# Kernel tuning notes

Hardware: AMD Instinct MI355X
Metric: run time of the kernel (lower is better)

## Reference

```python
import jax, jax.numpy as jnp
import numpy as np

N_DELTA, N_THETA, N_GAMMA = 64, 128, 512
N_TOTAL = N_DELTA + N_THETA + N_GAMMA  # 704
N_CLASSES = 1000
N_STEPS = 5
DT = 0.01
COUPLING = 2.0      # coupling_strength
PAC_DT = 0.3        # delta->theta phase-amplitude coupling depth
PAC_TG = 0.3        # theta->gamma phase-amplitude coupling depth
SPARSITY = 0.1      # PhaseToRateConverter sparsity (fraction of active units)
SHARP = 10.0        # softness of the 'soft' sparsification gate
TWO_PI = 2.0 * np.pi
B = 65536


def setup_inputs() -> dict:
    key = jax.random.key(0)
    k1, k2, k3, k4 = jax.random.split(key, 4)
    x = jax.random.normal(k1, (B, N_TOTAL), dtype=jnp.float32)
    # per-sample random initial phases in [0,1), scaled to [0,2pi) inside reference
    phase0 = jax.random.uniform(k2, (B, N_TOTAL), dtype=jnp.float32)
    W = jax.random.normal(k3, (N_CLASSES, N_TOTAL), dtype=jnp.float32) * 0.02
    b = jax.random.normal(k4, (N_CLASSES,), dtype=jnp.float32) * 0.02
    return {"x": x, "phase0": phase0, "W": W, "b": b}


def _kuramoto(phi):
    # mean-field within-band Kuramoto coupling: K * mean_j sin(phi_j - phi_i)
    S = jnp.mean(jnp.sin(phi), axis=-1, keepdims=True)
    C = jnp.mean(jnp.cos(phi), axis=-1, keepdims=True)
    return COUPLING * (S * jnp.cos(phi) - C * jnp.sin(phi))


def _mean_phase(phi):
    # circular mean phase of a band, shape (B,1)
    return jnp.arctan2(jnp.mean(jnp.sin(phi), axis=-1, keepdims=True),
                       jnp.mean(jnp.cos(phi), axis=-1, keepdims=True))


def _forward(x, phase0, W, b):
    freqs = jnp.concatenate([
        jnp.linspace(1.0, 4.0, N_DELTA),    # delta band Hz
        jnp.linspace(4.0, 8.0, N_THETA),    # theta band Hz
        jnp.linspace(30.0, 80.0, N_GAMMA),  # gamma band Hz
    ]).astype(x.dtype)
    phi = phase0 * TWO_PI                       # (B, N_TOTAL)
    amp = 1.0 + jnp.abs(x) * 0.01               # amplitude seeded by |x|*0.01 on unit base
    d = slice(0, N_DELTA)
    t = slice(N_DELTA, N_DELTA + N_THETA)
    g = slice(N_DELTA + N_THETA, N_TOTAL)

    def step(carry, _):
        phi, amp = carry
        dphi = TWO_PI * freqs + jnp.concatenate(
            [_kuramoto(phi[:, d]), _kuramoto(phi[:, t]), _kuramoto(phi[:, g])], axis=-1)
        psi_d = _mean_phase(phi[:, d])
        psi_t = _mean_phase(phi[:, t])
        # PAC: theta amplitude driven by delta phase, gamma amplitude by theta phase
        damp = jnp.concatenate([
            jnp.zeros_like(amp[:, d]),
            PAC_DT * amp[:, t] * jnp.cos(psi_d),
            PAC_TG * amp[:, g] * jnp.cos(psi_t),
        ], axis=-1)
        phi_new = jnp.mod(phi + DT * dphi, TWO_PI)
        amp_new = amp + DT * damp
        return (phi_new, amp_new), None

    (phi, amp), _ = jax.lax.scan(step, (phi, amp), None, length=N_STEPS)

    # PhaseToRateConverter, mode='soft': raw rate then soft top-(sparsity) gate
    raw = amp * 0.5 * (1.0 + jnp.cos(phi))                              # (B, N_TOTAL)
    thr = jnp.quantile(raw, 1.0 - SPARSITY, axis=-1, keepdims=True)    # per-sample threshold
    rate = raw * jax.nn.sigmoid((raw - thr) * SHARP)
    return rate @ W.T + b                                               # (B, N_CLASSES)


def reference(x, phase0, W, b):
    return _forward(x, phase0, W, b)
```

## Files before the change

### kernel.cpp

```cpp
#include <hip/hip_runtime.h>

#define NB 65536
#define NTOT 704
#define NCLS 1000
#define NPAD 1024
#define KDIM 704

typedef __attribute__((ext_vector_type(8))) short bf16x8;
typedef __attribute__((ext_vector_type(4))) float f32x4;
typedef __attribute__((ext_vector_type(2))) float f32x2;

#define WB_ELEMS (NPAD * KDIM)
#define LUT_DC_OFF (2u * (WB_ELEMS + 46137344u))
#define LUT_DS_OFF (LUT_DC_OFF + NTOT * 4u)

__device__ __forceinline__ f32x2 sp(float x) { return (f32x2){x, x}; }

template <int CTRL>
__device__ __forceinline__ float dpp_shuf(float v) {
  return __int_as_float(__builtin_amdgcn_update_dpp(0, __float_as_int(v), CTRL, 0xF, 0xF, true));
}
__device__ __forceinline__ float swz16(float v) {
  return __int_as_float(__builtin_amdgcn_ds_swizzle(__float_as_int(v), 0x401F));
}
__device__ __forceinline__ float wsum_f(float v) {
  v += dpp_shuf<0xB1>(v);
  v += dpp_shuf<0x4E>(v);
  v += dpp_shuf<0x141>(v);
  v += dpp_shuf<0x140>(v);
  v += swz16(v);
  v += __shfl_xor(v, 32, 64);
  return v;
}
__device__ __forceinline__ float wmax_f(float v) {
  v = fmaxf(v, dpp_shuf<0xB1>(v));
  v = fmaxf(v, dpp_shuf<0x4E>(v));
  v = fmaxf(v, dpp_shuf<0x141>(v));
  v = fmaxf(v, dpp_shuf<0x140>(v));
  v = fmaxf(v, swz16(v));
  v = fmaxf(v, __shfl_xor(v, 32, 64));
  return v;
}
__device__ __forceinline__ float wmin_f(float v) {
  v = fminf(v, dpp_shuf<0xB1>(v));
  v = fminf(v, dpp_shuf<0x4E>(v));
  v = fminf(v, dpp_shuf<0x141>(v));
  v = fminf(v, dpp_shuf<0x140>(v));
  v = fminf(v, swz16(v));
  v = fminf(v, __shfl_xor(v, 32, 64));
  return v;
}

__device__ __forceinline__ unsigned short f2bf(float v) {
  unsigned u = __float_as_uint(v);
  u = (u + 0x7FFFu + ((u >> 16) & 1u)) >> 16;
  return (unsigned short)u;
}

__global__ __launch_bounds__(256) void convw_kernel(const float* __restrict__ W,
                                                    unsigned short* __restrict__ Wb,
                                                    float* __restrict__ dcL,
                                                    float* __restrict__ dsL) {
  int i = blockIdx.x * 256 + threadIdx.x;
  if (i < NTOT) {
    float f;
    if (i < 64)       f = 1.0f + 3.0f * (float)i * (1.0f / 63.0f);
    else if (i < 192) f = 4.0f + 4.0f * (float)(i - 64) * (1.0f / 127.0f);
    else              f = 30.0f + 50.0f * (float)(i - 192) * (1.0f / 511.0f);
    const float rev = 0.01f * f;
    dcL[i] = __builtin_amdgcn_cosf(rev);
    dsL[i] = __builtin_amdgcn_sinf(rev);
  }
  if (i >= NPAD * KDIM) return;
  int n = i / KDIM;
  float v = (n < NCLS) ? W[i] : 0.0f;
  Wb[i] = f2bf(v);
}

__global__ __launch_bounds__(256) void sim_kernel(const float* __restrict__ x,
                                                  const float* __restrict__ p0,
                                                  const float* __restrict__ dcL,
                                                  const float* __restrict__ dsL,
                                                  unsigned short* __restrict__ rateb) {
  const int wave = threadIdx.x >> 6;
  const int lane = threadIdx.x & 63;
  const int sample = blockIdx.x * 4 + wave;
  const size_t base = (size_t)sample * NTOT;

  float sD, cD, ampD, dcD, dsD;
  f32x2 sPp[5], cPp[5], dc2[5], ds2[5], amp2[5];
  {
    const float p = p0[base + lane];
    sD = __builtin_amdgcn_sinf(p);
    cD = __builtin_amdgcn_cosf(p);
    ampD = fmaf(fabsf(x[base + lane]), 0.01f, 1.0f);
    dcD = dcL[lane]; dsD = dsL[lane];
  }
#pragma unroll
  for (int pr = 0; pr < 5; ++pr) {
    const int i0 = (1 + 2 * pr) * 64 + lane;
    const int i1 = i0 + 64;
    const float pa = p0[base + i0], pb = p0[base + i1];
    sPp[pr] = (f32x2){__builtin_amdgcn_sinf(pa), __builtin_amdgcn_sinf(pb)};
    cPp[pr] = (f32x2){__builtin_amdgcn_cosf(pa), __builtin_amdgcn_cosf(pb)};
    amp2[pr] = (f32x2){fmaf(fabsf(x[base + i0]), 0.01f, 1.0f),
                       fmaf(fabsf(x[base + i1]), 0.01f, 1.0f)};
    dc2[pr] = (f32x2){dcL[i0], dcL[i1]};
    ds2[pr] = (f32x2){dsL[i0], dsL[i1]};
  }

  float prodT = 1.0f, prodG = 1.0f;

#pragma unroll
  for (int st = 0; st < 5; ++st) {
    const float Sd = wsum_f(sD);
    const float Cd = wsum_f(cD);
    const float St = wsum_f(sPp[0].x + sPp[0].y);
    const float Ct = wsum_f(cPp[0].x + cPp[0].y);
    const f32x2 gs = (sPp[1] + sPp[2]) + (sPp[3] + sPp[4]);
    const f32x2 gc = (cPp[1] + cPp[2]) + (cPp[3] + cPp[4]);
    const float Sg = wsum_f(gs.x + gs.y);
    const float Cg = wsum_f(gc.x + gc.y);
    const float cpd = Cd * __builtin_amdgcn_rsqf(fmaf(Sd, Sd, Cd * Cd));
    const float cpt = Ct * __builtin_amdgcn_rsqf(fmaf(St, St, Ct * Ct));
    prodT *= fmaf(0.003f, cpd, 1.0f);
    prodG *= fmaf(0.003f, cpt, 1.0f);
    const float sdm = Sd * (0.02f / 64.0f),  cdm = Cd * (0.02f / 64.0f);
    const float stm = St * (0.02f / 128.0f), ctm = Ct * (0.02f / 128.0f);
    const float sgm = Sg * (0.02f / 512.0f), cgm = Cg * (0.02f / 512.0f);
    {
      const float eps = fmaf(-cdm, sD, sdm * cD);
      const float e2 = eps * eps;
      const float ce = fmaf(-0.5f, e2, 1.0f);
      const float cd_ = fmaf(-dsD, eps, dcD * ce);
      const float sd_ = fmaf(dcD, eps, dsD * ce);
      const float sn = fmaf(cD, sd_, sD * cd_);
      const float cn = fmaf(-sD, sd_, cD * cd_);
      sD = sn; cD = cn;
    }
#pragma unroll
    for (int pr = 0; pr < 5; ++pr) {
      const f32x2 Sm = sp(pr == 0 ? stm : sgm);
      const f32x2 Cm = sp(pr == 0 ? ctm : cgm);
      const f32x2 s2 = sPp[pr], c2 = cPp[pr];
      const f32x2 eps = Sm * c2 - Cm * s2;
      const f32x2 e2 = eps * eps;
      const f32x2 ce = sp(1.0f) - sp(0.5f) * e2;
      const f32x2 cosd = dc2[pr] * ce - ds2[pr] * eps;
      const f32x2 sind = ds2[pr] * ce + dc2[pr] * eps;
      sPp[pr] = s2 * cosd + c2 * sind;
      cPp[pr] = c2 * cosd - s2 * sind;
    }
  }

  float raw[11];
  unsigned kk[11];
  {
    const float h = 0.5f * ampD;
    raw[0] = fmaf(h, cD, h);
  }
  const float hT = 0.5f * prodT, hG = 0.5f * prodG;
#pragma unroll
  for (int pr = 0; pr < 5; ++pr) {
    const f32x2 h2 = amp2[pr] * sp(pr == 0 ? hT : hG);
    const f32x2 r2 = h2 * cPp[pr] + h2;
    raw[1 + 2 * pr] = r2.x;
    raw[2 + 2 * pr] = r2.y;
  }
#pragma unroll
  for (int e = 0; e < 11; ++e) kk[e] = (unsigned)(raw[e] * 8192.0f);

  unsigned pre = 0;
#pragma unroll
  for (int bit = 13; bit >= 0; --bit) {
    const unsigned u = pre | ((1u << bit) - 1u);
    int cnt = 0;
#pragma unroll
    for (int e = 0; e < 11; ++e) cnt += (int)__popcll(__ballot(kk[e] <= u));
    if (cnt < 633) pre |= (1u << bit);
  }

  int clt = 0, ceq = 0;
#pragma unroll
  for (int e = 0; e < 11; ++e) {
    clt += (int)__popcll(__ballot(kk[e] < pre));
    ceq += (int)__popcll(__ballot(kk[e] == pre));
  }

  const float qv = 0.9f * 703.0f;
  float thr;
  if (clt + ceq >= 634) {
    thr = ((float)pre + 0.5f) * (1.0f / 8192.0f);
  } else {
    float mx = -1.0f, mn = 3.0e38f;
#pragma unroll
    for (int e = 0; e < 11; ++e) {
      mx = fmaxf(mx, (kk[e] == pre) ? raw[e] : -1.0f);
      mn = fminf(mn, (kk[e] > pre) ? raw[e] : 3.0e38f);
    }
    const float S632 = wmax_f(mx);
    const float S633 = wmin_f(mn);
    thr = S632 * (633.0f - qv) + S633 * (qv - 632.0f);
  }

#pragma unroll
  for (int e = 0; e < 11; ++e) {
    const float r = raw[e];
    const float t = __expf((thr - r) * 10.0f);
    const float sg = __builtin_amdgcn_rcpf(1.0f + t);
    rateb[base + e * 64 + lane] = f2bf(r * sg);
  }
}

#define BM 128
#define BN 128
#define BK 64
#define NKT (KDIM / BK)

__device__ __forceinline__ void gload16(const unsigned short* g, unsigned short* l) {
  __builtin_amdgcn_global_load_lds((const __attribute__((address_space(1))) void*)g,
                                   (__attribute__((address_space(3))) void*)l,
                                   16, 0, 0);
}

__global__ __launch_bounds__(256) void gemm_kernel(const unsigned short* __restrict__ A,
                                                   const unsigned short* __restrict__ Bw,
                                                   const float* __restrict__ bias,
                                                   float* __restrict__ C) {
  __shared__ unsigned short lA[2][BM * BK];
  __shared__ unsigned short lB[2][BN * BK];
  const int tid  = threadIdx.x;
  const int wave = tid >> 6;
  const int lane = tid & 63;

  const int bid = blockIdx.x;
  const int swz = (bid & 7) * 512 + (bid >> 3);
  const int bm = swz >> 3;
  const int bn = swz & 7;

  const int wr = wave >> 1;
  const int wc = wave & 1;

  f32x4 acc[4][4];
#pragma unroll
  for (int i = 0; i < 4; ++i)
#pragma unroll
    for (int j = 0; j < 4; ++j) acc[i][j] = (f32x4){0.f, 0.f, 0.f, 0.f};

  const int lrow  = lane >> 3;
  const int lkblk = (((lane & 7) ^ lrow)) * 8;

  const unsigned short* Abase = A  + (size_t)(bm * BM) * KDIM;
  const unsigned short* Bbase = Bw + (size_t)(bn * BN) * KDIM;

#define STAGE(buf, kt)                                                          \
  {                                                                             \
    const int k0_ = (kt) * BK;                                                  \
    _Pragma("unroll")                                                           \
    for (int i_ = 0; i_ < 4; ++i_) {                                            \
      const int c_ = wave * 4 + i_;                                             \
      gload16(Abase + (size_t)(c_ * 8 + lrow) * KDIM + k0_ + lkblk,             \
              &lA[buf][c_ * 512]);                                              \
      gload16(Bbase + (size_t)(c_ * 8 + lrow) * KDIM + k0_ + lkblk,             \
              &lB[buf][c_ * 512]);                                              \
    }                                                                           \
  }

  STAGE(0, 0);
  __syncthreads();

  int buf = 0;
  for (int kt = 0; kt < NKT; ++kt) {
    if (kt < NKT - 1) STAGE(buf ^ 1, kt + 1);
#pragma unroll
    for (int ks = 0; ks < 2; ++ks) {
      bf16x8 av[4], bv[4];
      const int slot = 8 * ((((ks << 2) | (lane >> 4)) ^ (lane & 7)));
#pragma unroll
      for (int m = 0; m < 4; ++m) {
        const int r = wr * 64 + m * 16 + (lane & 15);
        av[m] = *(const bf16x8*)&lA[buf][r * BK + slot];
      }
#pragma unroll
      for (int n = 0; n < 4; ++n) {
        const int r = wc * 64 + n * 16 + (lane & 15);
        bv[n] = *(const bf16x8*)&lB[buf][r * BK + slot];
      }
#pragma unroll
      for (int m = 0; m < 4; ++m)
#pragma unroll
        for (int n = 0; n < 4; ++n)
          acc[m][n] = __builtin_amdgcn_mfma_f32_16x16x32_bf16(av[m], bv[n], acc[m][n], 0, 0, 0);
    }
    __syncthreads();
    buf ^= 1;
  }

  const int crow0 = bm * BM + wr * 64;
  const int ccol0 = bn * BN + wc * 64;
  const int rql = (lane >> 4) * 4;
  const int cl  = lane & 15;
#pragma unroll
  for (int n = 0; n < 4; ++n) {
    const int col = ccol0 + n * 16 + cl;
    if (col < NCLS) {
      const float bb = bias[col];
#pragma unroll
      for (int m = 0; m < 4; ++m) {
#pragma unroll
        for (int r = 0; r < 4; ++r) {
          const int row = crow0 + m * 16 + rql + r;
          C[(size_t)row * NCLS + col] = acc[m][n][r] + bb;
        }
      }
    }
  }
}

extern "C" void kernel_launch(void* const* d_in, const int* in_sizes, int n_in,
                              void* d_out, int out_size, void* d_ws, size_t ws_size,
                              hipStream_t stream) {
  const float* x    = (const float*)d_in[0];
  const float* p0   = (const float*)d_in[1];
  const float* W    = (const float*)d_in[2];
  const float* bias = (const float*)d_in[3];
  float* out = (float*)d_out;

  unsigned short* Wb    = (unsigned short*)d_ws;
  unsigned short* rateb = (unsigned short*)d_ws + WB_ELEMS;
  float* dcL = (float*)((char*)d_ws + LUT_DC_OFF);
  float* dsL = (float*)((char*)d_ws + LUT_DS_OFF);

  convw_kernel<<<dim3((NPAD * KDIM + 255) / 256), dim3(256), 0, stream>>>(W, Wb, dcL, dsL);
  sim_kernel<<<dim3(NB / 4), dim3(256), 0, stream>>>(x, p0, dcL, dsL, rateb);
  gemm_kernel<<<dim3((NB / BM) * (NPAD / BN)), dim3(256), 0, stream>>>(rateb, Wb, bias, out);
}
```

Before: 362.4 us.

## Software-pipeline GEMM main loop with register fragments and two-deep prefetch

Restructures the bf16 GEMM main loop so each iteration first reads all LDS fragments for both k-substeps into registers. It then frees that buffer with a barrier and issues the global-to-LDS loads for tile kt+2 into it, so those loads overlap the MFMA work. Hand-written s_waitcnt vmcnt/lgkmcnt and s_barrier instructions replace __syncthreads, and the last two tiles are peeled into an epilogue. In exchange, register pressure rises because twice as many fragments are held, and correctness now depends on the hand-placed wait counts.

```diff
diff --git a/kernel.cpp b/kernel.cpp
--- a/kernel.cpp
+++ b/kernel.cpp
@@ -223,12 +223,46 @@
                                    16, 0, 0);
 }
 
+struct Frags {
+  bf16x8 a[2][4];
+  bf16x8 b[2][4];
+};
+
+__device__ __forceinline__ void read_frags(Frags& f,
+                                           const unsigned short* la,
+                                           const unsigned short* lb,
+                                           int wr, int wc, int lane) {
+  const int l15 = lane & 15;
+  const int s0 = 8 * (((lane >> 4)) ^ (lane & 7));
+  const int s1 = 8 * ((4 | (lane >> 4)) ^ (lane & 7));
+#pragma unroll
+  for (int m = 0; m < 4; ++m) {
+    const int rA = (wr * 64 + m * 16 + l15) * BK;
+    const int rB = (wc * 64 + m * 16 + l15) * BK;
+    f.a[0][m] = *(const bf16x8*)&la[rA + s0];
+    f.a[1][m] = *(const bf16x8*)&la[rA + s1];
+    f.b[0][m] = *(const bf16x8*)&lb[rB + s0];
+    f.b[1][m] = *(const bf16x8*)&lb[rB + s1];
+  }
+}
+
+__device__ __forceinline__ void do_mfma(const Frags& f, f32x4 acc[4][4]) {
+#pragma unroll
+  for (int ks = 0; ks < 2; ++ks)
+#pragma unroll
+    for (int m = 0; m < 4; ++m)
+#pragma unroll
+      for (int n = 0; n < 4; ++n)
+        acc[m][n] = __builtin_amdgcn_mfma_f32_16x16x32_bf16(f.a[ks][m], f.b[ks][n],
+                                                            acc[m][n], 0, 0, 0);
+}
+
 __global__ __launch_bounds__(256) void gemm_kernel(const unsigned short* __restrict__ A,
                                                    const unsigned short* __restrict__ Bw,
                                                    const float* __restrict__ bias,
                                                    float* __restrict__ C) {
-  __shared__ unsigned short lA[2][BM * BK];
-  __shared__ unsigned short lB[2][BN * BK];
+  __shared__ __align__(16) unsigned short lA[2][BM * BK];
+  __shared__ __align__(16) unsigned short lB[2][BN * BK];
   const int tid  = threadIdx.x;
   const int wave = tid >> 6;
   const int lane = tid & 63;
@@ -267,34 +301,30 @@
   }
 
   STAGE(0, 0);
-  __syncthreads();
-
-  int buf = 0;
-  for (int kt = 0; kt < NKT; ++kt) {
-    if (kt < NKT - 1) STAGE(buf ^ 1, kt + 1);
-#pragma unroll
-    for (int ks = 0; ks < 2; ++ks) {
-      bf16x8 av[4], bv[4];
-      const int slot = 8 * ((((ks << 2) | (lane >> 4)) ^ (lane & 7)));
-#pragma unroll
-      for (int m = 0; m < 4; ++m) {
-        const int r = wr * 64 + m * 16 + (lane & 15);
-        av[m] = *(const bf16x8*)&lA[buf][r * BK + slot];
-      }
-#pragma unroll
-      for (int n = 0; n < 4; ++n) {
-        const int r = wc * 64 + n * 16 + (lane & 15);
-        bv[n] = *(const bf16x8*)&lB[buf][r * BK + slot];
-      }
-#pragma unroll
-      for (int m = 0; m < 4; ++m)
-#pragma unroll
-        for (int n = 0; n < 4; ++n)
-          acc[m][n] = __builtin_amdgcn_mfma_f32_16x16x32_bf16(av[m], bv[n], acc[m][n], 0, 0, 0);
-    }
-    __syncthreads();
-    buf ^= 1;
-  }
+  STAGE(1, 1);
+  asm volatile("s_waitcnt vmcnt(8)" ::: "memory");
+  asm volatile("s_barrier" ::: "memory");
+
+  Frags f;
+#pragma unroll 1
+  for (int kt = 0; kt < NKT - 2; ++kt) {
+    read_frags(f, lA[kt & 1], lB[kt & 1], wr, wc, lane);
+    asm volatile("s_waitcnt lgkmcnt(0)" ::: "memory");
+    asm volatile("s_barrier" ::: "memory");
+    STAGE(kt & 1, kt + 2);
+    do_mfma(f, acc);
+    asm volatile("s_waitcnt vmcnt(8)" ::: "memory");
+    asm volatile("s_barrier" ::: "memory");
+  }
+  read_frags(f, lA[1], lB[1], wr, wc, lane);
+  asm volatile("s_waitcnt lgkmcnt(0)" ::: "memory");
+  asm volatile("s_barrier" ::: "memory");
+  do_mfma(f, acc);
+  asm volatile("s_waitcnt vmcnt(0)" ::: "memory");
+  asm volatile("s_barrier" ::: "memory");
+  read_frags(f, lA[0], lB[0], wr, wc, lane);
+  asm volatile("s_waitcnt lgkmcnt(0)" ::: "memory");
+  do_mfma(f, acc);
 
   const int crow0 = bm * BM + wr * 64;
   const int ccol0 = bn * BN + wc * 64;
```

Result: faster. 343.7 us (-5.1%).
